# Performance work log

Hardware: AMD Instinct MI355X
Metric: run time of the kernel (lower is better)

Reference implementation:

```python
import jax, jax.numpy as jnp
import numpy as np
from functools import partial

T, B, IN, H, OUT = 8192, 1, 15, 1024, 15
NUM_LAYERS = 2
NUM_LINEAR = 2
SLOPE = 0.8  # LeakyReLU negative slope used by LinearCell


def leaky(x):
    return jnp.where(x >= 0, x, SLOPE * x)


def setup_inputs() -> dict:
    key = jax.random.key(0)
    ks = jax.random.split(key, 18)
    n = lambda k, shape, s: (jax.random.normal(k, shape, jnp.float32) * s)
    inp = {
        "x": jax.random.normal(ks[0], (T, B, IN), jnp.float32),
        # LSTM layer 0 (input -> hidden), gate order [i, f, g, o] as in PyTorch
        "W_ih0": n(ks[1], (4 * H, IN), 0.05),
        "W_hh0": n(ks[2], (4 * H, H), 0.02),
        "b_ih0": n(ks[3], (4 * H,), 0.02),
        "b_hh0": n(ks[4], (4 * H,), 0.02),
        # LSTM layer 1 (hidden -> hidden)
        "W_ih1": n(ks[5], (4 * H, H), 0.02),
        "W_hh1": n(ks[6], (4 * H, H), 0.02),
        "b_ih1": n(ks[7], (4 * H,), 0.02),
        "b_hh1": n(ks[8], (4 * H,), 0.02),
        # LinearSeq stack (num_linear LinearCells, H->H)
        "lin_W": n(ks[9], (NUM_LINEAR, H, H), 0.02),
        "lin_b": n(ks[10], (NUM_LINEAR, H), 0.02),
        # L1, L2 (H->H) and LOut (H->OUT)
        "W1": n(ks[11], (H, H), 0.02),
        "b1": n(ks[12], (H,), 0.02),
        "W2": n(ks[13], (H, H), 0.02),
        "b2": n(ks[14], (H,), 0.02),
        "Wo": n(ks[15], (OUT, H), 0.03),
        "bo": n(ks[16], (OUT,), 0.02),
        "future": 16,
    }
    return inp


def reference(x, W_ih0, W_hh0, b_ih0, b_hh0, W_ih1, W_hh1, b_ih1, b_hh1,
              lin_W, lin_b, W1, b1, W2, b2, Wo, bo, future):
    layer_params = [(W_ih0, W_hh0, b_ih0, b_hh0), (W_ih1, W_hh1, b_ih1, b_hh1)]

    def lstm_layers(h, c, inp):
        # h, c: [L, 1, H]; inp: [1, in_l]
        new_h, new_c = [], []
        for l, (Wih, Whh, bih, bhh) in enumerate(layer_params):
            gates = inp @ Wih.T + h[l] @ Whh.T + bih + bhh  # [1, 4H]
            i, f, g, o = jnp.split(gates, 4, axis=-1)
            cn = jax.nn.sigmoid(f) * c[l] + jax.nn.sigmoid(i) * jnp.tanh(g)
            hn = jax.nn.sigmoid(o) * jnp.tanh(cn)
            new_h.append(hn)
            new_c.append(cn)
            inp = hn
        return jnp.stack(new_h), jnp.stack(new_c), inp

    def mlp(h):
        # pointwise over leading dims; Dropout(0) == identity (eval)
        for l in range(NUM_LINEAR):
            h = leaky(h @ lin_W[l].T + lin_b[l])
        h = leaky(h @ W1.T + b1)
        h = leaky(h @ W2.T + b2)
        return leaky(h @ Wo.T + bo)

    h0 = jnp.zeros((NUM_LAYERS, 1, H), x.dtype)
    c0 = jnp.zeros((NUM_LAYERS, 1, H), x.dtype)

    def step(carry, xt):
        h, c = carry
        h, c, out = lstm_layers(h, c, xt)
        return (h, c), out

    (h, c), hs = jax.lax.scan(step, (h0, c0), x)  # hs: [T, 1, H]
    outs_seq = mlp(hs)                            # [T, 1, OUT] (vectorized over T)
    last = outs_seq[-1]                           # [1, OUT]

    def fstep(carry, _):
        h, c, out = carry
        h, c, hid = lstm_layers(h, c, out)
        out = mlp(hid)
        return (h, c, out), out

    (_, _, _), fouts = jax.lax.scan(fstep, (h, c, last), None, length=future)
    return jnp.concatenate([outs_seq, fouts], axis=0)  # [T+future, 1, OUT]
```

## Files before the change

### kernel.cpp

```cpp
#include <hip/hip_runtime.h>
#include <hip/hip_bf16.h>

#define TSTEPS 8192
#define HDIM   1024
#define FUT    16
#define RSLOT  8

typedef unsigned short bfu;
typedef __bf16 bf8v  __attribute__((ext_vector_type(8)));
typedef float  f32x4 __attribute__((ext_vector_type(4)));
typedef int    i32x4 __attribute__((ext_vector_type(4)));
typedef int    i32x2 __attribute__((ext_vector_type(2)));

__device__ __forceinline__ float u2lo(unsigned u){ return __uint_as_float(u << 16); }
__device__ __forceinline__ float u2hi(unsigned u){ return __uint_as_float(u & 0xffff0000u); }
__device__ __forceinline__ bfu f2bfu(float f){
  unsigned u = __float_as_uint(f);
  return (bfu)((u + 0x7fffu + ((u >> 16) & 1u)) >> 16);
}
__device__ __forceinline__ ushort4 pack4(float4 v){
  ushort4 p; p.x = f2bfu(v.x); p.y = f2bfu(v.y); p.z = f2bfu(v.z); p.w = f2bfu(v.w); return p;
}
__device__ __forceinline__ float leaky(float v){ return v >= 0.f ? v : 0.8f * v; }
__device__ __forceinline__ float sigm(float v){ return 1.f / (1.f + expf(-v)); }

__device__ __forceinline__ void st2c(void* p, float h, int tag){
  i32x2 v; v.x = __float_as_int(h); v.y = tag;
  asm volatile("global_store_dwordx2 %0, %1, off sc1" :: "v"(p), "v"(v) : "memory");
}

__device__ __forceinline__ void stage1024(const char* buf, int want, float* vs,
                                          int wv, int lane){
  const char* base = buf + (wv << 11) + (lane << 4);
  i32x4 q0, q1;
  for (;;) {
    asm volatile(
      "global_load_dwordx4 %0, %2, off sc1\n\t"
      "global_load_dwordx4 %1, %2, off offset:1024 sc1\n\t"
      "s_waitcnt vmcnt(0)"
      : "=&v"(q0), "=&v"(q1) : "v"(base) : "memory");
    if (q0.y == want && q0.w == want && q1.y == want && q1.w == want) break;
    __builtin_amdgcn_s_sleep(2);
  }
  int idx = (wv << 8) + (lane << 1);
  float2 f0 = {__int_as_float(q0.x), __int_as_float(q0.z)};
  float2 f1 = {__int_as_float(q1.x), __int_as_float(q1.z)};
  *(float2*)(vs + idx)       = f0;
  *(float2*)(vs + idx + 128) = f1;
}

__global__ __launch_bounds__(256, 1) void lstm_seq(
    const float* __restrict__ x,
    const float* __restrict__ Wih0, const float* __restrict__ Whh0,
    const float* __restrict__ bih0, const float* __restrict__ bhh0,
    const float* __restrict__ Wih1, const float* __restrict__ Whh1,
    const float* __restrict__ bih1, const float* __restrict__ bhh1,
    bfu* __restrict__ hsbf, char* __restrict__ hrec,
    float* __restrict__ c0s, float* __restrict__ c1s,
    float* __restrict__ h0f, float* __restrict__ h1f)
{
  __shared__ float hcat[2048];

  const int tid  = threadIdx.x;
  const int b    = blockIdx.x;
  const int wv   = tid >> 6;
  const int lane = tid & 63;
  const int u    = (b << 2) + wv;

  float w0[4][16], wa[4][16], wb[4][16];
  float wxr[4], bs0[4], bs1[4];
  #pragma unroll
  for (int g = 0; g < 4; ++g) {
    const size_t row = (size_t)((g << 10) + u);
    #pragma unroll
    for (int j = 0; j < 4; ++j) {
      *(float4*)&w0[g][j * 4] = *(const float4*)(Whh0 + row * 1024 + j * 256 + lane * 4);
      *(float4*)&wa[g][j * 4] = *(const float4*)(Wih1 + row * 1024 + j * 256 + lane * 4);
      *(float4*)&wb[g][j * 4] = *(const float4*)(Whh1 + row * 1024 + j * 256 + lane * 4);
    }
    wxr[g] = (lane < 15) ? Wih0[row * 15 + lane] : 0.f;
    bs0[g] = bih0[row] + bhh0[row];
    bs1[g] = bih1[row] + bhh1[row];
  }
  float cc0 = 0.f, hv0 = 0.f, cc1 = 0.f, hv1 = 0.f;

  if (lane == 0) {
    st2c(hrec + u * 8, 0.f, -1);
    st2c(hrec + 8192 + u * 8, 0.f, -1);
  }

  for (int t = 0; t <= TSTEPS; ++t) {
    const char* rec = hrec + (size_t)(t & (RSLOT - 1)) * 16384;
    const int want = t - 1;
    float xv = (lane < 15 && t < TSTEPS) ? x[t * 15 + lane] : 0.f;

    {
      const char* base = rec + (wv << 12) + (lane << 4);
      i32x4 q0, q1, q2, q3;
      for (;;) {
        asm volatile(
          "global_load_dwordx4 %0, %4, off sc1\n\t"
          "global_load_dwordx4 %1, %4, off offset:1024 sc1\n\t"
          "global_load_dwordx4 %2, %4, off offset:2048 sc1\n\t"
          "global_load_dwordx4 %3, %4, off offset:3072 sc1\n\t"
          "s_waitcnt vmcnt(0)"
          : "=&v"(q0), "=&v"(q1), "=&v"(q2), "=&v"(q3) : "v"(base) : "memory");
        if (q0.y == want && q0.w == want && q1.y == want && q1.w == want &&
            q2.y == want && q2.w == want && q3.y == want && q3.w == want) break;
        __builtin_amdgcn_s_sleep(2);
      }
      int idx = (wv << 9) + (lane << 1);
      float2 f0 = {__int_as_float(q0.x), __int_as_float(q0.z)};
      float2 f1 = {__int_as_float(q1.x), __int_as_float(q1.z)};
      float2 f2 = {__int_as_float(q2.x), __int_as_float(q2.z)};
      float2 f3 = {__int_as_float(q3.x), __int_as_float(q3.z)};
      *(float2*)(hcat + idx)       = f0;
      *(float2*)(hcat + idx + 128) = f1;
      *(float2*)(hcat + idx + 256) = f2;
      *(float2*)(hcat + idx + 384) = f3;
    }
    __syncthreads();

    float a0[4] = {0.f,0.f,0.f,0.f}, a1[4] = {0.f,0.f,0.f,0.f};
    #pragma unroll
    for (int j = 0; j < 4; ++j) {
      f32x4 h0r = *(const f32x4*)(hcat + j * 256 + lane * 4);
      f32x4 h1r = *(const f32x4*)(hcat + 1024 + j * 256 + lane * 4);
      #pragma unroll
      for (int m = 0; m < 4; ++m) {
        float h0v = h0r[m], h1v = h1r[m];
        #pragma unroll
        for (int g = 0; g < 4; ++g) {
          a0[g] = fmaf(w0[g][j * 4 + m], h0v, a0[g]);
          a1[g] = fmaf(wa[g][j * 4 + m], h0v, a1[g]);
          a1[g] = fmaf(wb[g][j * 4 + m], h1v, a1[g]);
        }
      }
    }
    #pragma unroll
    for (int g = 0; g < 4; ++g) a0[g] = fmaf(wxr[g], xv, a0[g]);
    #pragma unroll
    for (int off = 32; off; off >>= 1) {
      #pragma unroll
      for (int g = 0; g < 4; ++g) {
        a0[g] += __shfl_xor(a0[g], off);
        a1[g] += __shfl_xor(a1[g], off);
      }
    }
    float h1out = 0.f;
    if (t < TSTEPS) {
      float ii = sigm(a0[0] + bs0[0]), ff = sigm(a0[1] + bs0[1]);
      float gv = tanhf(a0[2] + bs0[2]), oo = sigm(a0[3] + bs0[3]);
      cc0 = ff * cc0 + ii * gv;
      hv0 = oo * tanhf(cc0);
    }
    if (t > 0) {
      float ii = sigm(a1[0] + bs1[0]), ff = sigm(a1[1] + bs1[1]);
      float gv = tanhf(a1[2] + bs1[2]), oo = sigm(a1[3] + bs1[3]);
      cc1 = ff * cc1 + ii * gv;
      hv1 = oo * tanhf(cc1);
      h1out = hv1;
    }
    if (lane == 0) {
      if (t < TSTEPS) {
        char* nrec = hrec + (size_t)((t + 1) & (RSLOT - 1)) * 16384;
        st2c(nrec + u * 8, hv0, t);
        st2c(nrec + 8192 + u * 8, h1out, t);
      }
      if (t > 0) hsbf[(size_t)(t - 1) * HDIM + u] = f2bfu(hv1);
    }
  }
  if (lane == 0) {
    c0s[u] = cc0; h0f[u] = hv0;
    c1s[u] = cc1; h1f[u] = hv1;
  }
}

__global__ void cast_w(const float* __restrict__ linW, const float* __restrict__ W1m,
                       const float* __restrict__ W2m, bfu* __restrict__ wbf)
{
  int e4 = (blockIdx.x * 256 + threadIdx.x) * 4;
  int seg = e4 >> 20, off = e4 & 1048575;
  const float* src = (seg == 0) ? linW + off
                   : (seg == 1) ? linW + 1048576 + off
                   : (seg == 2) ? W1m + off : W2m + off;
  float4 v = *(const float4*)src;
  *(ushort4*)(wbf + e4) = pack4(v);
}

__global__ __launch_bounds__(256, 1) void mlp_gemm(
    const bfu* __restrict__ A, const bfu* __restrict__ Bw,
    const float* __restrict__ bias, bfu* __restrict__ Out)
{
  __shared__ bfu At[128 * 40];
  __shared__ bfu Bt[128 * 40];
  const int tid = threadIdx.x;
  const int bm = blockIdx.x * 128, bn = blockIdx.y * 128;
  const int wv = tid >> 6, lane = tid & 63;
  const int wm = (wv & 1) * 64, wn = (wv >> 1) * 64;
  const int m16 = lane & 15, q = lane >> 4;
  f32x4 acc[4][4];
  #pragma unroll
  for (int i = 0; i < 4; ++i)
    #pragma unroll
    for (int j = 0; j < 4; ++j) { f32x4 z = {0.f,0.f,0.f,0.f}; acc[i][j] = z; }

  for (int kt = 0; kt < 1024; kt += 32) {
    __syncthreads();
    #pragma unroll
    for (int i = 0; i < 2; ++i) {
      int idx = tid + i * 256;
      int r = idx >> 2, ch = idx & 3;
      *(uint4*)(At + r * 40 + ch * 8) = *(const uint4*)(A  + (size_t)(bm + r) * 1024 + kt + ch * 8);
      *(uint4*)(Bt + r * 40 + ch * 8) = *(const uint4*)(Bw + (size_t)(bn + r) * 1024 + kt + ch * 8);
    }
    __syncthreads();
    bf8v af[4], bfv[4];
    #pragma unroll
    for (int i = 0; i < 4; ++i) af[i]  = *(const bf8v*)(const void*)(At + (wm + i * 16 + m16) * 40 + q * 8);
    #pragma unroll
    for (int j = 0; j < 4; ++j) bfv[j] = *(const bf8v*)(const void*)(Bt + (wn + j * 16 + m16) * 40 + q * 8);
    #pragma unroll
    for (int i = 0; i < 4; ++i)
      #pragma unroll
      for (int j = 0; j < 4; ++j)
        acc[i][j] = __builtin_amdgcn_mfma_f32_16x16x32_bf16(af[i], bfv[j], acc[i][j], 0, 0, 0);
  }
  #pragma unroll
  for (int j = 0; j < 4; ++j) {
    int col = bn + wn + j * 16 + m16;
    float bv = bias[col];
    #pragma unroll
    for (int i = 0; i < 4; ++i) {
      #pragma unroll
      for (int r = 0; r < 4; ++r) {
        int row = bm + wm + i * 16 + q * 4 + r;
        float v = leaky(acc[i][j][r] + bv);
        Out[(size_t)row * 1024 + col] = f2bfu(v);
      }
    }
  }
}

__global__ void wo_ker(const bfu* __restrict__ Hb, const float* __restrict__ Wo,
                       const float* __restrict__ bo, float* __restrict__ dout,
                       char* __restrict__ pbo)
{
  int tid = threadIdx.x;
  int t = blockIdx.x * 16 + (tid >> 4);
  int o = tid & 15;
  if (o == 15) return;
  const bfu* hr = Hb + (size_t)t * 1024;
  const float* wr = Wo + (size_t)o * 1024;
  float acc = 0.f;
  for (int k = 0; k < 1024; k += 8) {
    uint4 hc = *(const uint4*)(hr + k);
    float4 w0 = *(const float4*)(wr + k);
    float4 w1 = *(const float4*)(wr + k + 4);
    acc = fmaf(u2lo(hc.x), w0.x, acc); acc = fmaf(u2hi(hc.x), w0.y, acc);
    acc = fmaf(u2lo(hc.y), w0.z, acc); acc = fmaf(u2hi(hc.y), w0.w, acc);
    acc = fmaf(u2lo(hc.z), w1.x, acc); acc = fmaf(u2hi(hc.z), w1.y, acc);
    acc = fmaf(u2lo(hc.w), w1.z, acc); acc = fmaf(u2hi(hc.w), w1.w, acc);
  }
  acc = leaky(acc + bo[o]);
  dout[t * 15 + o] = acc;
  if (t == 8191) st2c(pbo + o * 8, acc, -1);
}

__device__ __forceinline__ float rowdot1024(const float* __restrict__ W,
                                            const float* __restrict__ v, int lane){
  float acc = 0.f;
  #pragma unroll
  for (int p = 0; p < 4; ++p) {
    int k = p * 256 + lane * 4;
    float4 w = *(const float4*)(W + k);
    float4 h = *(const float4*)(v + k);
    acc = fmaf(w.x, h.x, acc); acc = fmaf(w.y, h.y, acc);
    acc = fmaf(w.z, h.z, acc); acc = fmaf(w.w, h.w, acc);
  }
  #pragma unroll
  for (int off = 32; off; off >>= 1) acc += __shfl_xor(acc, off);
  return acc;
}

__global__ __launch_bounds__(256, 1) void future_seq(
    const float* __restrict__ Wih0, const float* __restrict__ Whh0,
    const float* __restrict__ bih0, const float* __restrict__ bhh0,
    const float* __restrict__ Wih1, const float* __restrict__ Whh1,
    const float* __restrict__ bih1, const float* __restrict__ bhh1,
    const float* __restrict__ linW, const float* __restrict__ linb,
    const float* __restrict__ W1m, const float* __restrict__ b1v,
    const float* __restrict__ W2m, const float* __restrict__ b2v,
    const float* __restrict__ Wo, const float* __restrict__ bo,
    const float* __restrict__ h0f, const float* __restrict__ h1f,
    const float* __restrict__ c0s, const float* __restrict__ c1s,
    char* __restrict__ pb0, char* __restrict__ pb1,
    char* __restrict__ pv1, char* __restrict__ pv2,
    char* __restrict__ pv3, char* __restrict__ pv4,
    char* __restrict__ pbo, float* __restrict__ dout)
{
  __shared__ float vs[1024];
  __shared__ float vs2[1024];
  __shared__ float xsf[16];
  const int tid = threadIdx.x, b = blockIdx.x, wv = tid >> 6, lane = tid & 63;
  const int unit = (b << 2) + wv;
  float c0 = c0s[unit], c1 = c1s[unit];

  if (lane == 0) {
    st2c(pb0 + unit * 8, h0f[unit], -1);
    st2c(pb1 + unit * 8, h1f[unit], -1);
  }

  for (int s = 0; s < FUT; ++s) {
    const int cur = (s & 1) * 8192, nxt = ((s + 1) & 1) * 8192;
    stage1024(pb0 + cur, s - 1, vs, wv, lane);
    if (tid < 15) {
      const char* p = pbo + tid * 8;
      i32x2 q;
      for (;;) {
        asm volatile("global_load_dwordx2 %0, %1, off sc1\n\ts_waitcnt vmcnt(0)"
                     : "=&v"(q) : "v"(p) : "memory");
        if (q.y == s - 1) break;
        __builtin_amdgcn_s_sleep(2);
      }
      xsf[tid] = __int_as_float(q.x);
    }
    __syncthreads();
    float a[4];
    #pragma unroll
    for (int g = 0; g < 4; ++g)
      a[g] = rowdot1024(Whh0 + (size_t)((g << 10) + unit) * 1024, vs, lane);
    {
      float gg[4];
      #pragma unroll
      for (int g = 0; g < 4; ++g) {
        int R = (g << 10) + unit;
        float s15 = 0.f;
        #pragma unroll
        for (int k = 0; k < 15; ++k) s15 = fmaf(Wih0[R * 15 + k], xsf[k], s15);
        gg[g] = a[g] + s15 + bih0[R] + bhh0[R];
      }
      float ii = sigm(gg[0]), ff = sigm(gg[1]), gv = tanhf(gg[2]), oo = sigm(gg[3]);
      c0 = ff * c0 + ii * gv;
      if (lane == 0) st2c(pb0 + nxt + unit * 8, oo * tanhf(c0), s);
    }
    stage1024(pb0 + nxt, s, vs, wv, lane);
    stage1024(pb1 + cur, s - 1, vs2, wv, lane);
    __syncthreads();
    #pragma unroll
    for (int g = 0; g < 4; ++g) {
      int R = (g << 10) + unit;
      float acc = 0.f;
      #pragma unroll
      for (int p = 0; p < 4; ++p) {
        int k = p * 256 + lane * 4;
        float4 w = *(const float4*)(Wih1 + (size_t)R * 1024 + k);
        float4 h = *(const float4*)(vs + k);
        acc = fmaf(w.x, h.x, acc); acc = fmaf(w.y, h.y, acc);
        acc = fmaf(w.z, h.z, acc); acc = fmaf(w.w, h.w, acc);
        float4 w2 = *(const float4*)(Whh1 + (size_t)R * 1024 + k);
        float4 h2 = *(const float4*)(vs2 + k);
        acc = fmaf(w2.x, h2.x, acc); acc = fmaf(w2.y, h2.y, acc);
        acc = fmaf(w2.z, h2.z, acc); acc = fmaf(w2.w, h2.w, acc);
      }
      #pragma unroll
      for (int off = 32; off; off >>= 1) acc += __shfl_xor(acc, off);
      a[g] = acc;
    }
    {
      float gg[4];
      #pragma unroll
      for (int g = 0; g < 4; ++g) { int R = (g << 10) + unit; gg[g] = a[g] + bih1[R] + bhh1[R]; }
      float ii = sigm(gg[0]), ff = sigm(gg[1]), gv = tanhf(gg[2]), oo = sigm(gg[3]);
      c1 = ff * c1 + ii * gv;
      if (lane == 0) st2c(pb1 + nxt + unit * 8, oo * tanhf(c1), s);
    }
    {
      const char* vin[4] = {pb1 + nxt, pv1, pv2, pv3};
      const int vtag[4]  = {s, s, s, s};
      char* vo[4] = {pv1, pv2, pv3, pv4};
      #pragma unroll
      for (int l = 0; l < 4; ++l) {
        const float* Wd = (l == 0) ? linW : (l == 1) ? linW + 1048576 : (l == 2) ? W1m : W2m;
        const float* bd = (l == 0) ? linb : (l == 1) ? linb + 1024 : (l == 2) ? b1v : b2v;
        stage1024(vin[l], vtag[l], vs, wv, lane);
        __syncthreads();
        float acc = rowdot1024(Wd + (size_t)unit * 1024, vs, lane);
        if (lane == 0) st2c(vo[l] + unit * 8, leaky(acc + bd[unit]), s);
        __syncthreads();
      }
    }
    if (b == 0) {
      stage1024(pv4, s, vs, wv, lane);
      __syncthreads();
      for (int o = wv; o < 15; o += 4) {
        float acc = rowdot1024(Wo + (size_t)o * 1024, vs, lane);
        if (lane == 0) {
          float r = leaky(acc + bo[o]);
          dout[(8192 + s) * 15 + o] = r;
          st2c(pbo + o * 8, r, s);
        }
      }
      __syncthreads();
    }
  }
}

extern "C" void kernel_launch(void* const* d_in, const int* in_sizes, int n_in,
                              void* d_out, int out_size, void* d_ws, size_t ws_size,
                              hipStream_t stream)
{
  (void)in_sizes; (void)n_in; (void)out_size; (void)ws_size;
  const float* x    = (const float*)d_in[0];
  const float* Wih0 = (const float*)d_in[1];
  const float* Whh0 = (const float*)d_in[2];
  const float* bih0 = (const float*)d_in[3];
  const float* bhh0 = (const float*)d_in[4];
  const float* Wih1 = (const float*)d_in[5];
  const float* Whh1 = (const float*)d_in[6];
  const float* bih1 = (const float*)d_in[7];
  const float* bhh1 = (const float*)d_in[8];
  const float* linW = (const float*)d_in[9];
  const float* linb = (const float*)d_in[10];
  const float* W1m  = (const float*)d_in[11];
  const float* b1v  = (const float*)d_in[12];
  const float* W2m  = (const float*)d_in[13];
  const float* b2v  = (const float*)d_in[14];
  const float* Wo   = (const float*)d_in[15];
  const float* bo   = (const float*)d_in[16];
  float* dout = (float*)d_out;
  char*  ws   = (char*)d_ws;

  bfu*  hsbf = (bfu*)(ws);
  bfu*  ping = (bfu*)(ws + (size_t)16777216);
  bfu*  wbf  = (bfu*)(ws + (size_t)33554432);
  char* hrec = ws + (size_t)41943040;
  char* pb0  = hrec + 131072;
  char* pb1  = pb0 + 16384;
  char* pv1  = pb1 + 16384;
  char* pv2  = pv1 + 8192;
  char* pv3  = pv2 + 8192;
  char* pv4  = pv3 + 8192;
  char* pbo  = pv4 + 8192;
  float* c0s = (float*)(pbo + 256);
  float* c1s = c0s + 1024;
  float* h0f = c1s + 1024;
  float* h1f = h0f + 1024;

  cast_w<<<dim3(4096), dim3(256), 0, stream>>>(linW, W1m, W2m, wbf);

  lstm_seq<<<dim3(256), dim3(256), 0, stream>>>(
      x, Wih0, Whh0, bih0, bhh0, Wih1, Whh1, bih1, bhh1,
      hsbf, hrec, c0s, c1s, h0f, h1f);

  dim3 gg(64, 8), bb(256);
  mlp_gemm<<<gg, bb, 0, stream>>>(hsbf, wbf,           linb,        ping);
  mlp_gemm<<<gg, bb, 0, stream>>>(ping, wbf + 1048576, linb + 1024, hsbf);
  mlp_gemm<<<gg, bb, 0, stream>>>(hsbf, wbf + 2097152, b1v,         ping);
  mlp_gemm<<<gg, bb, 0, stream>>>(ping, wbf + 3145728, b2v,         hsbf);

  wo_ker<<<dim3(512), dim3(256), 0, stream>>>(hsbf, Wo, bo, dout, pbo);

  future_seq<<<dim3(256), dim3(256), 0, stream>>>(
      Wih0, Whh0, bih0, bhh0, Wih1, Whh1, bih1, bhh1,
      linW, linb, W1m, b1v, W2m, b2v, Wo, bo,
      h0f, h1f, c0s, c1s, pb0, pb1, pv1, pv2, pv3, pv4, pbo, dout);
}
```

Before: 38.95 ms.

## Replace all-to-all tag polling with hierarchical aggregator flags in LSTM recurrence

Instead of every block polling all 2048 tagged h values for each timestep, 16 aggregator waves each watch a 1KB chunk and publish a readiness flag replicated into 8 copies. Each block then polls 16 flags and does one unconditional load of the full state. The aim is to cut global polling traffic and contention on the critical path of the sequential recurrence, at the cost of an extra hop of latency through the aggregators. Correctness relies on store ordering between the h writes and the flag writes under sc1 semantics.

Measured after the change: 39.09 ms. Within noise of the previous version (+0.4%).

```diff
diff --git a/kernel.cpp b/kernel.cpp
--- a/kernel.cpp
+++ b/kernel.cpp
@@ -27,6 +27,15 @@
 __device__ __forceinline__ void st2c(void* p, float h, int tag){
   i32x2 v; v.x = __float_as_int(h); v.y = tag;
   asm volatile("global_store_dwordx2 %0, %1, off sc1" :: "v"(p), "v"(v) : "memory");
+}
+__device__ __forceinline__ void stic(int* p, int v){
+  asm volatile("global_store_dword %0, %1, off sc1" :: "v"(p), "v"(v) : "memory");
+}
+__device__ __forceinline__ int ldic(const int* p){
+  int v;
+  asm volatile("global_load_dword %0, %1, off sc1\n\ts_waitcnt vmcnt(0)"
+               : "=v"(v) : "v"(p) : "memory");
+  return v;
 }
 
 __device__ __forceinline__ void stage1024(const char* buf, int want, float* vs,
@@ -55,7 +64,7 @@
     const float* __restrict__ bih0, const float* __restrict__ bhh0,
     const float* __restrict__ Wih1, const float* __restrict__ Whh1,
     const float* __restrict__ bih1, const float* __restrict__ bhh1,
-    bfu* __restrict__ hsbf, char* __restrict__ hrec,
+    bfu* __restrict__ hsbf, char* __restrict__ hrec, char* __restrict__ tags,
     float* __restrict__ c0s, float* __restrict__ c1s,
     float* __restrict__ h0f, float* __restrict__ h1f)
 {
@@ -66,6 +75,7 @@
   const int wv   = tid >> 6;
   const int lane = tid & 63;
   const int u    = (b << 2) + wv;
+  const bool agg = (b < 16) && (wv == 0);
 
   float w0[4][16], wa[4][16], wb[4][16];
   float wxr[4], bs0[4], bs1[4];
@@ -90,25 +100,41 @@
   }
 
   for (int t = 0; t <= TSTEPS; ++t) {
-    const char* rec = hrec + (size_t)(t & (RSLOT - 1)) * 16384;
+    const int slot = t & (RSLOT - 1);
+    const char* rec = hrec + (size_t)slot * 16384;
     const int want = t - 1;
     float xv = (lane < 15 && t < TSTEPS) ? x[t * 15 + lane] : 0.f;
 
+    if (agg) {
+      const char* abase = rec + b * 1024 + (lane << 4);
+      i32x4 q;
+      for (;;) {
+        asm volatile("global_load_dwordx4 %0, %1, off sc1\n\ts_waitcnt vmcnt(0)"
+                     : "=&v"(q) : "v"(abase) : "memory");
+        if (q.y == want && q.w == want) break;
+        __builtin_amdgcn_s_sleep(1);
+      }
+      if (lane < 8)
+        stic((int*)(tags + slot * 512 + lane * 64 + b * 4), want);
+    }
     {
-      const char* base = rec + (wv << 12) + (lane << 4);
+      const int* tl = (const int*)(tags + slot * 512 + (b & 7) * 64);
+      for (;;) {
+        int v = ldic(tl + (lane & 15));
+        if (__ballot(v == want) == ~0ull) break;
+        __builtin_amdgcn_s_sleep(1);
+      }
+    }
+    {
+      const char* sbase = rec + (wv << 12) + (lane << 4);
       i32x4 q0, q1, q2, q3;
-      for (;;) {
-        asm volatile(
-          "global_load_dwordx4 %0, %4, off sc1\n\t"
-          "global_load_dwordx4 %1, %4, off offset:1024 sc1\n\t"
-          "global_load_dwordx4 %2, %4, off offset:2048 sc1\n\t"
-          "global_load_dwordx4 %3, %4, off offset:3072 sc1\n\t"
-          "s_waitcnt vmcnt(0)"
-          : "=&v"(q0), "=&v"(q1), "=&v"(q2), "=&v"(q3) : "v"(base) : "memory");
-        if (q0.y == want && q0.w == want && q1.y == want && q1.w == want &&
-            q2.y == want && q2.w == want && q3.y == want && q3.w == want) break;
-        __builtin_amdgcn_s_sleep(2);
-      }
+      asm volatile(
+        "global_load_dwordx4 %0, %4, off sc1\n\t"
+        "global_load_dwordx4 %1, %4, off offset:1024 sc1\n\t"
+        "global_load_dwordx4 %2, %4, off offset:2048 sc1\n\t"
+        "global_load_dwordx4 %3, %4, off offset:3072 sc1\n\t"
+        "s_waitcnt vmcnt(0)"
+        : "=&v"(q0), "=&v"(q1), "=&v"(q2), "=&v"(q3) : "v"(sbase) : "memory");
       int idx = (wv << 9) + (lane << 1);
       float2 f0 = {__int_as_float(q0.x), __int_as_float(q0.z)};
       float2 f1 = {__int_as_float(q1.x), __int_as_float(q1.z)};
@@ -377,13 +403,12 @@
     }
     {
       const char* vin[4] = {pb1 + nxt, pv1, pv2, pv3};
-      const int vtag[4]  = {s, s, s, s};
       char* vo[4] = {pv1, pv2, pv3, pv4};
       #pragma unroll
       for (int l = 0; l < 4; ++l) {
         const float* Wd = (l == 0) ? linW : (l == 1) ? linW + 1048576 : (l == 2) ? W1m : W2m;
         const float* bd = (l == 0) ? linb : (l == 1) ? linb + 1024 : (l == 2) ? b1v : b2v;
-        stage1024(vin[l], vtag[l], vs, wv, lane);
+        stage1024(vin[l], s, vs, wv, lane);
         __syncthreads();
         float acc = rowdot1024(Wd + (size_t)unit * 1024, vs, lane);
         if (lane == 0) st2c(vo[l] + unit * 8, leaky(acc + bd[unit]), s);
@@ -435,7 +460,8 @@
   bfu*  ping = (bfu*)(ws + (size_t)16777216);
   bfu*  wbf  = (bfu*)(ws + (size_t)33554432);
   char* hrec = ws + (size_t)41943040;
-  char* pb0  = hrec + 131072;
+  char* tags = hrec + 131072;
+  char* pb0  = tags + 4096;
   char* pb1  = pb0 + 16384;
   char* pv1  = pb1 + 16384;
   char* pv2  = pv1 + 8192;
@@ -451,7 +477,7 @@
 
   lstm_seq<<<dim3(256), dim3(256), 0, stream>>>(
       x, Wih0, Whh0, bih0, bhh0, Wih1, Whh1, bih1, bhh1,
-      hsbf, hrec, c0s, c1s, h0f, h1f);
+      hsbf, hrec, tags, c0s, c1s, h0f, h1f);
 
   dim3 gg(64, 8), bb(256);
   mlp_gemm<<<gg, bb, 0, stream>>>(hsbf, wbf,           linb,        ping);
```

## Halve persistent LSTM grid to 128 blocks of 512 threads with per-slot polling

Applied to the files above, without the earlier changes.

The persistent recurrent kernel now runs 128 blocks of 8 waves instead of 256 blocks of 4 waves, with each wave still owning one hidden unit. The spin-wait that gathers the previous hidden state now spreads its loads across all threads, two 16-byte slots per thread. Each thread re-polls only the slots that are not yet ready and exits when a wave ballot says everything has arrived. Publishing h0 and h1 and writing the bf16 output are split across lanes 0, 1 and 2. The aim is to cut the number of blocks polling global memory each step and the per-thread polling load. In exchange it adds a second __syncthreads per timestep to protect the shared buffer, and each block carries more register pressure at 512 threads.

Result: slower. 49.97 ms (+28.3%).

```diff
diff --git a/kernel.cpp b/kernel.cpp
--- a/kernel.cpp
+++ b/kernel.cpp
@@ -49,7 +49,7 @@
   *(float2*)(vs + idx + 128) = f1;
 }
 
-__global__ __launch_bounds__(256, 1) void lstm_seq(
+__global__ __launch_bounds__(512, 1) void lstm_seq(
     const float* __restrict__ x,
     const float* __restrict__ Wih0, const float* __restrict__ Whh0,
     const float* __restrict__ bih0, const float* __restrict__ bhh0,
@@ -65,7 +65,7 @@
   const int b    = blockIdx.x;
   const int wv   = tid >> 6;
   const int lane = tid & 63;
-  const int u    = (b << 2) + wv;
+  const int u    = (b << 3) + wv;
 
   float w0[4][16], wa[4][16], wb[4][16];
   float wxr[4], bs0[4], bs1[4];
@@ -84,10 +84,7 @@
   }
   float cc0 = 0.f, hv0 = 0.f, cc1 = 0.f, hv1 = 0.f;
 
-  if (lane == 0) {
-    st2c(hrec + u * 8, 0.f, -1);
-    st2c(hrec + 8192 + u * 8, 0.f, -1);
-  }
+  if (lane < 2) st2c(hrec + lane * 8192 + u * 8, 0.f, -1);
 
   for (int t = 0; t <= TSTEPS; ++t) {
     const char* rec = hrec + (size_t)(t & (RSLOT - 1)) * 16384;
@@ -95,29 +92,27 @@
     float xv = (lane < 15 && t < TSTEPS) ? x[t * 15 + lane] : 0.f;
 
     {
-      const char* base = rec + (wv << 12) + (lane << 4);
-      i32x4 q0, q1, q2, q3;
+      const char* sbase = rec + tid * 32;
+      i32x4 q0, q1;
+      bool k0 = false, k1 = false;
       for (;;) {
-        asm volatile(
-          "global_load_dwordx4 %0, %4, off sc1\n\t"
-          "global_load_dwordx4 %1, %4, off offset:1024 sc1\n\t"
-          "global_load_dwordx4 %2, %4, off offset:2048 sc1\n\t"
-          "global_load_dwordx4 %3, %4, off offset:3072 sc1\n\t"
-          "s_waitcnt vmcnt(0)"
-          : "=&v"(q0), "=&v"(q1), "=&v"(q2), "=&v"(q3) : "v"(base) : "memory");
-        if (q0.y == want && q0.w == want && q1.y == want && q1.w == want &&
-            q2.y == want && q2.w == want && q3.y == want && q3.w == want) break;
-        __builtin_amdgcn_s_sleep(2);
-      }
-      int idx = (wv << 9) + (lane << 1);
+        if (!k0)
+          asm volatile("global_load_dwordx4 %0, %1, off sc1"
+                       : "=v"(q0) : "v"(sbase) : "memory");
+        if (!k1)
+          asm volatile("global_load_dwordx4 %0, %1, off offset:16 sc1"
+                       : "=v"(q1) : "v"(sbase) : "memory");
+        asm volatile("s_waitcnt vmcnt(0)" : "+v"(q0), "+v"(q1) :: "memory");
+        k0 = (q0.y == want) && (q0.w == want);
+        k1 = (q1.y == want) && (q1.w == want);
+        if (__ballot(!(k0 && k1)) == 0ull) break;
+        __builtin_amdgcn_s_sleep(1);
+      }
+      int idx = tid * 4;
       float2 f0 = {__int_as_float(q0.x), __int_as_float(q0.z)};
       float2 f1 = {__int_as_float(q1.x), __int_as_float(q1.z)};
-      float2 f2 = {__int_as_float(q2.x), __int_as_float(q2.z)};
-      float2 f3 = {__int_as_float(q3.x), __int_as_float(q3.z)};
-      *(float2*)(hcat + idx)       = f0;
-      *(float2*)(hcat + idx + 128) = f1;
-      *(float2*)(hcat + idx + 256) = f2;
-      *(float2*)(hcat + idx + 384) = f3;
+      *(float2*)(hcat + idx)     = f0;
+      *(float2*)(hcat + idx + 2) = f1;
     }
     __syncthreads();
 
@@ -137,6 +132,7 @@
         }
       }
     }
+    __syncthreads();
     #pragma unroll
     for (int g = 0; g < 4; ++g) a0[g] = fmaf(wxr[g], xv, a0[g]);
     #pragma unroll
@@ -161,14 +157,13 @@
       hv1 = oo * tanhf(cc1);
       h1out = hv1;
     }
-    if (lane == 0) {
-      if (t < TSTEPS) {
-        char* nrec = hrec + (size_t)((t + 1) & (RSLOT - 1)) * 16384;
-        st2c(nrec + u * 8, hv0, t);
-        st2c(nrec + 8192 + u * 8, h1out, t);
-      }
-      if (t > 0) hsbf[(size_t)(t - 1) * HDIM + u] = f2bfu(hv1);
-    }
+    if (lane < 2 && t < TSTEPS) {
+      char* nrec = hrec + (size_t)((t + 1) & (RSLOT - 1)) * 16384;
+      float val = (lane == 0) ? hv0 : h1out;
+      st2c(nrec + lane * 8192 + u * 8, val, t);
+    }
+    if (lane == 2 && t > 0)
+      hsbf[(size_t)(t - 1) * HDIM + u] = f2bfu(hv1);
   }
   if (lane == 0) {
     c0s[u] = cc0; h0f[u] = hv0;
@@ -377,13 +372,12 @@
     }
     {
       const char* vin[4] = {pb1 + nxt, pv1, pv2, pv3};
-      const int vtag[4]  = {s, s, s, s};
       char* vo[4] = {pv1, pv2, pv3, pv4};
       #pragma unroll
       for (int l = 0; l < 4; ++l) {
         const float* Wd = (l == 0) ? linW : (l == 1) ? linW + 1048576 : (l == 2) ? W1m : W2m;
         const float* bd = (l == 0) ? linb : (l == 1) ? linb + 1024 : (l == 2) ? b1v : b2v;
-        stage1024(vin[l], vtag[l], vs, wv, lane);
+        stage1024(vin[l], s, vs, wv, lane);
         __syncthreads();
         float acc = rowdot1024(Wd + (size_t)unit * 1024, vs, lane);
         if (lane == 0) st2c(vo[l] + unit * 8, leaky(acc + bd[unit]), s);
@@ -449,7 +443,7 @@
 
   cast_w<<<dim3(4096), dim3(256), 0, stream>>>(linW, W1m, W2m, wbf);
 
-  lstm_seq<<<dim3(256), dim3(256), 0, stream>>>(
+  lstm_seq<<<dim3(128), dim3(512), 0, stream>>>(
       x, Wih0, Whh0, bih0, bhh0, Wih1, Whh1, bih1, bhh1,
       hsbf, hrec, c0s, c1s, h0f, h1f);
 
```
